# Kernel tuning notes

Measured on AMD Instinct MI355X. Metric: run time of the kernel, lower is better.

Reference implementation:

```python
import jax, jax.numpy as jnp
import numpy as np

S = 1024   # speakers_per_batch
U = 64     # utterances_per_speaker
D = 256    # embedding_size
EPS = 1e-5


def setup_inputs() -> dict:
    key = jax.random.key(0)
    k1, = jax.random.split(key, 1)
    return {
        "output_of_model": jax.random.normal(k1, (S * U, D), dtype=jnp.float32),
        "similarity_weight": jnp.array([10.0], dtype=jnp.float32),
        "similarity_bias": jnp.array([-5.0], dtype=jnp.float32),
        "speakers_per_batch": S,
        "utterances_per_speaker": U,
    }


def reference(output_of_model, similarity_weight, similarity_bias,
              speakers_per_batch, utterances_per_speaker):
    s, u = speakers_per_batch, utterances_per_speaker
    embeds = output_of_model.reshape(s, u, -1)                      # [S,U,D]

    # inclusive centroids (mean over utterances, L2-normalized with +eps)
    c_incl = jnp.mean(embeds, axis=1)                               # [S,D]
    c_incl = c_incl / (jnp.linalg.norm(c_incl, axis=-1, keepdims=True) + EPS)

    # exclusive centroids (leave-one-out mean, L2-normalized with +eps)
    c_excl = (jnp.sum(embeds, axis=1, keepdims=True) - embeds) / (u - 1)  # [S,U,D]
    c_excl = c_excl / (jnp.linalg.norm(c_excl, axis=-1, keepdims=True) + EPS)

    # normalized embeddings (original normalizes embeds inside the loop)
    e_n = embeds / (jnp.linalg.norm(embeds, axis=-1, keepdims=True) + EPS)

    # off-diagonal: cosine(embed[i,u], incl centroid[j]); diagonal: excl centroid
    sim_incl = jnp.einsum('sud,jd->suj', e_n, c_incl)               # [S,U,S]
    sim_excl = jnp.sum(e_n * c_excl, axis=-1)                       # [S,U]
    diag = jnp.eye(s, dtype=bool)[:, None, :]                       # [S,1,S]
    sim = jnp.where(diag, sim_excl[:, :, None], sim_incl)           # [S,U,S]

    sim = sim * similarity_weight + similarity_bias                 # scaled logits

    logits = sim.reshape(s * u, s)
    targets = jnp.repeat(jnp.arange(s), u)                          # ground truth
    logp = jax.nn.log_softmax(logits, axis=-1)
    loss = -jnp.mean(jnp.take_along_axis(logp, targets[:, None], axis=-1))
    return loss
```

## Files before the change

kernel.cpp:

```cpp
#include <hip/hip_runtime.h>

#define SPK 1024
#define UTT 64
#define DIM 256
#define EPSV 1e-5f
#define NROW (SPK * UTT)

typedef __attribute__((ext_vector_type(8))) short short8;
typedef __attribute__((ext_vector_type(4))) float f32x4;

__device__ __forceinline__ unsigned short f2bf(float f) {
    unsigned int u = __builtin_bit_cast(unsigned int, f);
    u += 0x7fffu + ((u >> 16) & 1u);
    return (unsigned short)(u >> 16);
}

__global__ __launch_bounds__(256)
void k_prep(const float* __restrict__ x,
            unsigned short* __restrict__ cincl,
            unsigned short* __restrict__ en,
            float* __restrict__ texcl,
            const float* __restrict__ wp, const float* __restrict__ bp) {
    __shared__ float4 sc4[256];
    __shared__ float4 cs4[64];
    __shared__ float sccs;
    int s = blockIdx.x, tid = threadIdx.x;
    int dq = tid & 63, ug = tid >> 6;
    const float4* x4 = (const float4*)(x + (size_t)s * UTT * DIM);

    float4 p = {0.f, 0.f, 0.f, 0.f};
#pragma unroll
    for (int i = 0; i < 16; ++i) {
        float4 v = x4[(ug * 16 + i) * 64 + dq];
        p.x += v.x; p.y += v.y; p.z += v.z; p.w += v.w;
    }
    sc4[tid] = p;
    __syncthreads();
    if (tid < 64) {
        float4 a = sc4[dq], b2 = sc4[64 + dq], c = sc4[128 + dq], d = sc4[192 + dq];
        float4 cs = {a.x + b2.x + c.x + d.x, a.y + b2.y + c.y + d.y,
                     a.z + b2.z + c.z + d.z, a.w + b2.w + c.w + d.w};
        cs4[dq] = cs;
        float s2 = cs.x * cs.x + cs.y * cs.y + cs.z * cs.z + cs.w * cs.w;
#pragma unroll
        for (int o = 1; o < 64; o <<= 1) s2 += __shfl_xor(s2, o);
        if (tid == 0) sccs = s2;
        float inv = 1.f / (sqrtf(s2) + UTT * EPSV);
        ushort4 ob = {f2bf(cs.x * inv), f2bf(cs.y * inv),
                      f2bf(cs.z * inv), f2bf(cs.w * inv)};
        *(ushort4*)(cincl + (size_t)s * DIM + dq * 4) = ob;
    }
    __syncthreads();
    float scc = sccs;
    float w = wp[0], b = bp[0];

    int row = tid >> 2, sub = tid & 3;
    const float4* xr = x4 + row * 64;
    float4 xv[16];
    float sx = 0.f, sc = 0.f;
#pragma unroll
    for (int i = 0; i < 16; ++i) {
        float4 v = xr[i * 4 + sub];
        float4 cv = cs4[i * 4 + sub];
        xv[i] = v;
        sx += v.x * v.x + v.y * v.y + v.z * v.z + v.w * v.w;
        sc += v.x * cv.x + v.y * cv.y + v.z * cv.z + v.w * cv.w;
    }
    sx += __shfl_xor(sx, 1); sx += __shfl_xor(sx, 2);
    sc += __shfl_xor(sc, 1); sc += __shfl_xor(sc, 2);
    float nx = sqrtf(sx);
    float inv = 1.f / (nx + EPSV);
    unsigned short* er = en + (size_t)(s * UTT + row) * DIM;
#pragma unroll
    for (int i = 0; i < 16; ++i) {
        ushort4 ob = {f2bf(xv[i].x * inv), f2bf(xv[i].y * inv),
                      f2bf(xv[i].z * inv), f2bf(xv[i].w * inv)};
        *(ushort4*)(er + (i * 4 + sub) * 4) = ob;
    }
    if (sub == 0) {
        float num = sc - sx;
        float e2 = fmaxf(scc - 2.f * sc + sx, 0.f);
        float sim = num / ((nx + EPSV) * (sqrtf(e2) + (UTT - 1) * EPSV));
        texcl[s * UTT + row] = fmaf(sim, w, b);
    }
}

__global__ __launch_bounds__(256, 1)
void k_main(const unsigned short* __restrict__ en,
            const unsigned short* __restrict__ cincl,
            const float* __restrict__ texcl,
            const float* __restrict__ wp, const float* __restrict__ bp,
            float* __restrict__ out) {
    __shared__ unsigned short Bs[2][32 * 512];
    int tid = threadIdx.x, wave = tid >> 6, lane = tid & 63;
    int quad = lane >> 4, lx = lane & 15;
    int sw = blockIdx.x * 4 + wave;
    float w = wp[0], b = bp[0];
    float M = fabsf(w) * 1.0625f + b;

    auto stage = [&](int c, int buf) {
#pragma unroll
        for (int i = 0; i < 8; ++i) {
            int p = wave * 8 + i;
            int nt = p >> 3, kt = p & 7;
            const unsigned short* g = cincl +
                (size_t)(c * 64 + nt * 16 + lx) * DIM + kt * 32 + quad * 8;
            __builtin_amdgcn_global_load_lds(
                (const __attribute__((address_space(1))) void*)g,
                (__attribute__((address_space(3))) void*)(&Bs[buf][p * 512]), 16, 0, 0);
        }
    };

    stage(0, 0);

    const unsigned short* abase = en + (size_t)sw * UTT * DIM;
    short8 af[4][8];
#pragma unroll
    for (int mt = 0; mt < 4; ++mt)
#pragma unroll
        for (int kt = 0; kt < 8; ++kt)
            af[mt][kt] = *(const short8*)(abase + (mt * 16 + lx) * DIM + kt * 32 + quad * 8);

    float l[16];
#pragma unroll
    for (int i = 0; i < 16; ++i) l[i] = 0.f;

    for (int c = 0; c < 16; ++c) {
        int buf = c & 1;
        __syncthreads();
        if (c < 15) stage(c + 1, buf ^ 1);
        int dnt = (sw - c * 64) >> 4;
#pragma unroll
        for (int nt = 0; nt < 4; ++nt) {
            short8 bf[8];
#pragma unroll
            for (int kt = 0; kt < 8; ++kt)
                bf[kt] = *(const short8*)(&Bs[buf][(nt * 8 + kt) * 512 + lane * 8]);
            f32x4 aA[4] = {{0.f,0.f,0.f,0.f},{0.f,0.f,0.f,0.f},
                           {0.f,0.f,0.f,0.f},{0.f,0.f,0.f,0.f}};
            f32x4 aB[4] = {{0.f,0.f,0.f,0.f},{0.f,0.f,0.f,0.f},
                           {0.f,0.f,0.f,0.f},{0.f,0.f,0.f,0.f}};
#pragma unroll
            for (int kt = 0; kt < 4; ++kt) {
                aA[0] = __builtin_amdgcn_mfma_f32_16x16x32_bf16(af[0][kt], bf[kt], aA[0], 0, 0, 0);
                aA[1] = __builtin_amdgcn_mfma_f32_16x16x32_bf16(af[1][kt], bf[kt], aA[1], 0, 0, 0);
                aA[2] = __builtin_amdgcn_mfma_f32_16x16x32_bf16(af[2][kt], bf[kt], aA[2], 0, 0, 0);
                aA[3] = __builtin_amdgcn_mfma_f32_16x16x32_bf16(af[3][kt], bf[kt], aA[3], 0, 0, 0);
                aB[0] = __builtin_amdgcn_mfma_f32_16x16x32_bf16(af[0][kt+4], bf[kt+4], aB[0], 0, 0, 0);
                aB[1] = __builtin_amdgcn_mfma_f32_16x16x32_bf16(af[1][kt+4], bf[kt+4], aB[1], 0, 0, 0);
                aB[2] = __builtin_amdgcn_mfma_f32_16x16x32_bf16(af[2][kt+4], bf[kt+4], aB[2], 0, 0, 0);
                aB[3] = __builtin_amdgcn_mfma_f32_16x16x32_bf16(af[3][kt+4], bf[kt+4], aB[3], 0, 0, 0);
            }
#pragma unroll
            for (int mt = 0; mt < 4; ++mt)
#pragma unroll
                for (int r = 0; r < 4; ++r) {
                    float v = fmaf(aA[mt][r] + aB[mt][r], w, b);
                    l[mt * 4 + r] += __expf(v - M);
                }
            if (nt == dnt) {
#pragma unroll
                for (int mt = 0; mt < 4; ++mt)
#pragma unroll
                    for (int r = 0; r < 4; ++r) {
                        float v = fmaf(aA[mt][r] + aB[mt][r], w, b);
                        float e = __expf(v - M);
                        if (lx == (sw & 15)) l[mt * 4 + r] -= e;
                    }
            }
        }
    }

#pragma unroll
    for (int o = 1; o < 16; o <<= 1)
#pragma unroll
        for (int i = 0; i < 16; ++i) l[i] += __shfl_xor(l[i], o);

    float contrib = 0.f;
    if (lx == 0) {
#pragma unroll
        for (int mt = 0; mt < 4; ++mt)
#pragma unroll
            for (int r = 0; r < 4; ++r) {
                int row = mt * 16 + quad * 4 + r;
                float tex = texcl[sw * UTT + row];
                float lsum = l[mt * 4 + r] + __expf(tex - M);
                contrib += (M + __logf(lsum)) - tex;
            }
    }
#pragma unroll
    for (int o = 1; o < 64; o <<= 1) contrib += __shfl_xor(contrib, o);
    if (lane == 0) atomicAdd(out, contrib * (1.f / NROW));
}

extern "C" void kernel_launch(void* const* d_in, const int* in_sizes, int n_in,
                              void* d_out, int out_size, void* d_ws, size_t ws_size,
                              hipStream_t stream) {
    const float* x  = (const float*)d_in[0];
    const float* wp = (const float*)d_in[1];
    const float* bp = (const float*)d_in[2];
    char* ws = (char*)d_ws;
    unsigned short* cincl = (unsigned short*)ws;
    float* texcl          = (float*)(ws + (1u << 19));
    unsigned short* en    = (unsigned short*)(ws + (1u << 20));
    float* out = (float*)d_out;

    hipMemsetAsync(d_out, 0, sizeof(float), stream);
    k_prep<<<SPK, 256, 0, stream>>>(x, cincl, en, texcl, wp, bp);
    k_main<<<SPK / 4, 256, 0, stream>>>(en, cincl, texcl, wp, bp, out);
}
```

Before: 169.7 us.

## Split each speaker's columns across waves and launch one block per speaker

Reassigns k_main so that each block handles a single speaker, with its four waves each covering a quarter of the centroid columns. Per-row partial exp sums are combined through shared memory before the log-sum. Launch bounds are raised to two blocks per CU, and the exponent now uses exp2 with the weight, bias and max folded into one fma. This quadruples grid size to improve occupancy and latency hiding. In exchange, each speaker's A fragments are loaded by every wave, and total centroid staging traffic grows fourfold.

Result: slower. 193.0 us (+13.8%).

```diff
diff --git a/kernel.cpp b/kernel.cpp
--- a/kernel.cpp
+++ b/kernel.cpp
@@ -5,6 +5,7 @@
 #define DIM 256
 #define EPSV 1e-5f
 #define NROW (SPK * UTT)
+#define LOG2E 1.44269504f
 
 typedef __attribute__((ext_vector_type(8))) short short8;
 typedef __attribute__((ext_vector_type(4))) float f32x4;
@@ -85,35 +86,38 @@
     }
 }
 
-__global__ __launch_bounds__(256, 1)
+__global__ __launch_bounds__(256, 2)
 void k_main(const unsigned short* __restrict__ en,
             const unsigned short* __restrict__ cincl,
             const float* __restrict__ texcl,
             const float* __restrict__ wp, const float* __restrict__ bp,
             float* __restrict__ out) {
     __shared__ unsigned short Bs[2][32 * 512];
+    __shared__ float sl[4][UTT];
     int tid = threadIdx.x, wave = tid >> 6, lane = tid & 63;
     int quad = lane >> 4, lx = lane & 15;
-    int sw = blockIdx.x * 4 + wave;
+    int s = blockIdx.x;
+    int col0 = wave * 256;
     float w = wp[0], b = bp[0];
-    float M = fabsf(w) * 1.0625f + b;
+    float M  = fabsf(w) * 1.0625f + b;
+    float wl = w * LOG2E;
+    float bl = (b - M) * LOG2E;
 
     auto stage = [&](int c, int buf) {
 #pragma unroll
-        for (int i = 0; i < 8; ++i) {
-            int p = wave * 8 + i;
-            int nt = p >> 3, kt = p & 7;
+        for (int kt = 0; kt < 8; ++kt) {
             const unsigned short* g = cincl +
-                (size_t)(c * 64 + nt * 16 + lx) * DIM + kt * 32 + quad * 8;
+                (size_t)(col0 + c * 16 + lx) * DIM + kt * 32 + quad * 8;
             __builtin_amdgcn_global_load_lds(
                 (const __attribute__((address_space(1))) void*)g,
-                (__attribute__((address_space(3))) void*)(&Bs[buf][p * 512]), 16, 0, 0);
+                (__attribute__((address_space(3))) void*)(&Bs[buf][(wave * 8 + kt) * 512]),
+                16, 0, 0);
         }
     };
 
     stage(0, 0);
 
-    const unsigned short* abase = en + (size_t)sw * UTT * DIM;
+    const unsigned short* abase = en + (size_t)s * UTT * DIM;
     short8 af[4][8];
 #pragma unroll
     for (int mt = 0; mt < 4; ++mt)
@@ -124,50 +128,46 @@
     float l[16];
 #pragma unroll
     for (int i = 0; i < 16; ++i) l[i] = 0.f;
+
+    int dc  = (s - col0) >> 4;
+    int dlx = s & 15;
 
     for (int c = 0; c < 16; ++c) {
         int buf = c & 1;
         __syncthreads();
         if (c < 15) stage(c + 1, buf ^ 1);
-        int dnt = (sw - c * 64) >> 4;
-#pragma unroll
-        for (int nt = 0; nt < 4; ++nt) {
-            short8 bf[8];
-#pragma unroll
-            for (int kt = 0; kt < 8; ++kt)
-                bf[kt] = *(const short8*)(&Bs[buf][(nt * 8 + kt) * 512 + lane * 8]);
-            f32x4 aA[4] = {{0.f,0.f,0.f,0.f},{0.f,0.f,0.f,0.f},
-                           {0.f,0.f,0.f,0.f},{0.f,0.f,0.f,0.f}};
-            f32x4 aB[4] = {{0.f,0.f,0.f,0.f},{0.f,0.f,0.f,0.f},
-                           {0.f,0.f,0.f,0.f},{0.f,0.f,0.f,0.f}};
-#pragma unroll
-            for (int kt = 0; kt < 4; ++kt) {
-                aA[0] = __builtin_amdgcn_mfma_f32_16x16x32_bf16(af[0][kt], bf[kt], aA[0], 0, 0, 0);
-                aA[1] = __builtin_amdgcn_mfma_f32_16x16x32_bf16(af[1][kt], bf[kt], aA[1], 0, 0, 0);
-                aA[2] = __builtin_amdgcn_mfma_f32_16x16x32_bf16(af[2][kt], bf[kt], aA[2], 0, 0, 0);
-                aA[3] = __builtin_amdgcn_mfma_f32_16x16x32_bf16(af[3][kt], bf[kt], aA[3], 0, 0, 0);
-                aB[0] = __builtin_amdgcn_mfma_f32_16x16x32_bf16(af[0][kt+4], bf[kt+4], aB[0], 0, 0, 0);
-                aB[1] = __builtin_amdgcn_mfma_f32_16x16x32_bf16(af[1][kt+4], bf[kt+4], aB[1], 0, 0, 0);
-                aB[2] = __builtin_amdgcn_mfma_f32_16x16x32_bf16(af[2][kt+4], bf[kt+4], aB[2], 0, 0, 0);
-                aB[3] = __builtin_amdgcn_mfma_f32_16x16x32_bf16(af[3][kt+4], bf[kt+4], aB[3], 0, 0, 0);
-            }
+        short8 bf[8];
+#pragma unroll
+        for (int kt = 0; kt < 8; ++kt)
+            bf[kt] = *(const short8*)(&Bs[buf][(wave * 8 + kt) * 512 + lane * 8]);
+        f32x4 aA[4] = {{0.f,0.f,0.f,0.f},{0.f,0.f,0.f,0.f},
+                       {0.f,0.f,0.f,0.f},{0.f,0.f,0.f,0.f}};
+        f32x4 aB[4] = {{0.f,0.f,0.f,0.f},{0.f,0.f,0.f,0.f},
+                       {0.f,0.f,0.f,0.f},{0.f,0.f,0.f,0.f}};
+#pragma unroll
+        for (int kt = 0; kt < 4; ++kt) {
+            aA[0] = __builtin_amdgcn_mfma_f32_16x16x32_bf16(af[0][kt], bf[kt], aA[0], 0, 0, 0);
+            aA[1] = __builtin_amdgcn_mfma_f32_16x16x32_bf16(af[1][kt], bf[kt], aA[1], 0, 0, 0);
+            aA[2] = __builtin_amdgcn_mfma_f32_16x16x32_bf16(af[2][kt], bf[kt], aA[2], 0, 0, 0);
+            aA[3] = __builtin_amdgcn_mfma_f32_16x16x32_bf16(af[3][kt], bf[kt], aA[3], 0, 0, 0);
+            aB[0] = __builtin_amdgcn_mfma_f32_16x16x32_bf16(af[0][kt+4], bf[kt+4], aB[0], 0, 0, 0);
+            aB[1] = __builtin_amdgcn_mfma_f32_16x16x32_bf16(af[1][kt+4], bf[kt+4], aB[1], 0, 0, 0);
+            aB[2] = __builtin_amdgcn_mfma_f32_16x16x32_bf16(af[2][kt+4], bf[kt+4], aB[2], 0, 0, 0);
+            aB[3] = __builtin_amdgcn_mfma_f32_16x16x32_bf16(af[3][kt+4], bf[kt+4], aB[3], 0, 0, 0);
+        }
+#pragma unroll
+        for (int mt = 0; mt < 4; ++mt)
+#pragma unroll
+            for (int r = 0; r < 4; ++r)
+                l[mt * 4 + r] += exp2f(fmaf(aA[mt][r] + aB[mt][r], wl, bl));
+        if (c == dc) {
 #pragma unroll
             for (int mt = 0; mt < 4; ++mt)
 #pragma unroll
                 for (int r = 0; r < 4; ++r) {
-                    float v = fmaf(aA[mt][r] + aB[mt][r], w, b);
-                    l[mt * 4 + r] += __expf(v - M);
+                    float e = exp2f(fmaf(aA[mt][r] + aB[mt][r], wl, bl));
+                    if (lx == dlx) l[mt * 4 + r] -= e;
                 }
-            if (nt == dnt) {
-#pragma unroll
-                for (int mt = 0; mt < 4; ++mt)
-#pragma unroll
-                    for (int r = 0; r < 4; ++r) {
-                        float v = fmaf(aA[mt][r] + aB[mt][r], w, b);
-                        float e = __expf(v - M);
-                        if (lx == (sw & 15)) l[mt * 4 + r] -= e;
-                    }
-            }
         }
     }
 
@@ -175,22 +175,23 @@
     for (int o = 1; o < 16; o <<= 1)
 #pragma unroll
         for (int i = 0; i < 16; ++i) l[i] += __shfl_xor(l[i], o);
-
-    float contrib = 0.f;
-    if (lx == 0) {
+    if (lx == 0)
 #pragma unroll
         for (int mt = 0; mt < 4; ++mt)
 #pragma unroll
-            for (int r = 0; r < 4; ++r) {
-                int row = mt * 16 + quad * 4 + r;
-                float tex = texcl[sw * UTT + row];
-                float lsum = l[mt * 4 + r] + __expf(tex - M);
-                contrib += (M + __logf(lsum)) - tex;
-            }
-    }
-#pragma unroll
-    for (int o = 1; o < 64; o <<= 1) contrib += __shfl_xor(contrib, o);
-    if (lane == 0) atomicAdd(out, contrib * (1.f / NROW));
+            for (int r = 0; r < 4; ++r)
+                sl[wave][mt * 16 + quad * 4 + r] = l[mt * 4 + r];
+    __syncthreads();
+
+    if (wave == 0) {
+        float lt = sl[0][lane] + sl[1][lane] + sl[2][lane] + sl[3][lane];
+        float tex = texcl[s * UTT + lane];
+        float lsum = lt + exp2f((tex - M) * LOG2E);
+        float contrib = (M + __logf(lsum)) - tex;
+#pragma unroll
+        for (int o = 1; o < 64; o <<= 1) contrib += __shfl_xor(contrib, o);
+        if (lane == 0) atomicAdd(out, contrib * (1.f / NROW));
+    }
 }
 
 extern "C" void kernel_launch(void* const* d_in, const int* in_sizes, int n_in,
@@ -207,5 +208,5 @@
 
     hipMemsetAsync(d_out, 0, sizeof(float), stream);
     k_prep<<<SPK, 256, 0, stream>>>(x, cincl, en, texcl, wp, bp);
-    k_main<<<SPK / 4, 256, 0, stream>>>(en, cincl, texcl, wp, bp, out);
-}
+    k_main<<<SPK, 256, 0, stream>>>(en, cincl, texcl, wp, bp, out);
+}
```
